# Kernel optimization log

Measured on AMD Instinct MI355X. Metric: run time of the kernel, lower is better.

## Reference

```python
import jax, jax.numpy as jnp
import numpy as np

NB_HEAD = 8
SIZE_PER_HEAD = 32
KEY_SIZE = 32
RATE = 2


def extract_seq_patches(x, kernel_size, rate):
    # x: [B, N, d] -> [B, N, kernel_size, d], dilated local windows (stride=rate)
    B, N, d = x.shape
    k_size = kernel_size + (rate - 1) * (kernel_size - 1)
    p_right = (k_size - 1) // 2
    p_left = k_size - 1 - p_right
    xp = jnp.pad(x, ((0, 0), (p_left, p_right), (0, 0)))
    xs = [xp[:, i:i + N] for i in range(0, k_size, rate)]  # kernel_size slices
    return jnp.stack(xs, axis=2)


def setup_inputs() -> dict:
    key = jax.random.key(0)
    k1, k2, k3 = jax.random.split(key, 3)
    B, S, D = 4, 2046, 256
    x = jax.random.normal(k1, (B, S, D), dtype=jnp.float32)
    # scale like nn.Linear init so softmax logits are well-conditioned
    W = jax.random.normal(k2, (D, NB_HEAD * SIZE_PER_HEAD), dtype=jnp.float32) / np.sqrt(D)
    b = jax.random.normal(k3, (NB_HEAD * SIZE_PER_HEAD,), dtype=jnp.float32) * 0.01
    return {"x": x, "W": W, "b": b}


def reference(x, W, b):
    rate, heads, dk, dv = RATE, NB_HEAD, KEY_SIZE, SIZE_PER_HEAD
    B, S, D = x.shape
    pad_len = rate - S % rate
    xp = jnp.pad(x, ((0, 0), (0, pad_len), (0, 0)))
    N = S + pad_len
    m = N // rate
    qkv = xp @ W + b                 # same Linear used for Q, K, V in the original
    Q = K = V = qkv                  # [B, N, heads*dk]
    ksz = 1 + 2 * (rate - 1)
    kwp = extract_seq_patches(K, ksz, rate)   # [B, N, ksz, H*dk]
    vwp = extract_seq_patches(V, ksz, rate)
    qw = Q.reshape(B, m, rate, heads, dk).transpose(0, 3, 2, 1, 4)   # [B,H,r,m,dk]
    kw = K.reshape(B, m, rate, heads, dk).transpose(0, 3, 2, 1, 4)
    vw = V.reshape(B, m, rate, heads, dv).transpose(0, 3, 2, 1, 4)
    kwp = kwp.reshape(B, m, rate, ksz, heads, dk).transpose(0, 4, 2, 1, 3, 5)  # [B,H,r,m,ksz,dk]
    vwp = vwp.reshape(B, m, rate, ksz, heads, dv).transpose(0, 4, 2, 1, 3, 5)
    scale = 1.0 / np.sqrt(dk).astype(np.float32)
    # strided scores; original transposes the last two dims (a.permute(0,1,2,4,3))
    a = jnp.einsum('bhrid,bhrjd->bhrji', qw, kw) * scale             # [B,H,r,m,m]
    # local-window scores: qw (as length-1 query) against dilated patches
    ap = jnp.einsum('bhrid,bhrikd->bhrik', qw, kwp) * scale          # [B,H,r,m,ksz]
    A = jax.nn.softmax(jnp.concatenate([a, ap], axis=-1), axis=-1)
    a, ap = A[..., :m], A[..., m:]
    o1 = jnp.einsum('bhrij,bhrjd->bhrid', a, vw)                     # [B,H,r,m,dv]
    o2 = jnp.einsum('bhrik,bhrikd->bhrid', ap, vwp)
    o = (o1 + o2).transpose(0, 3, 2, 1, 4).reshape(B, N, heads * dv)
    return o[:, :-pad_len]
```

## Files before the change

### kernel.cpp

```cpp
#include <hip/hip_runtime.h>
#include <stdint.h>
#include <stddef.h>

#define NB_HEAD 8
#define DHEAD   32
#define B_      4
#define S_      2046
#define N_      2048
#define M_      1024
#define D_      256

#define WT_S    264

typedef __attribute__((ext_vector_type(8))) short short8;
typedef __attribute__((ext_vector_type(4))) float f32x4;

__device__ __forceinline__ void bf2x2(uint32_t u, float& lo, float& hi) {
    union { uint32_t i; float f; } a, b;
    a.i = u << 16;
    b.i = u & 0xffff0000u;
    lo = a.f; hi = b.f;
}
__device__ __forceinline__ uint16_t f2bf(float f) {
    union { float f; uint32_t i; } v; v.f = f;
    uint32_t u = v.i;
    u += 0x7fffu + ((u >> 16) & 1u);
    return (uint16_t)(u >> 16);
}
__device__ __forceinline__ short8 ld_frag(const uint16_t* p) {
    union { uint4 u; short8 s; } v;
    v.u = *(const uint4*)p;
    return v.s;
}
__device__ __forceinline__ void unp8(short8 v, float* f) {
    union { short8 s; uint32_t u[4]; } x; x.s = v;
    #pragma unroll
    for (int k = 0; k < 4; ++k) bf2x2(x.u[k], f[2*k], f[2*k+1]);
}
__device__ __forceinline__ uint32_t pkbf(uint32_t hi, uint32_t lo) {
    return __builtin_amdgcn_perm(hi, lo, 0x07060302u);
}

__global__ __launch_bounds__(512) void proj_kernel(
    const float* __restrict__ x, const float* __restrict__ W,
    const float* __restrict__ bias,
    uint16_t* __restrict__ qkv, uint16_t* __restrict__ qkvT)
{
    __shared__ __align__(16) uint16_t WtL[64 * WT_S];
    __shared__ float    mrgP[4][16][64];
    __shared__ uint16_t Tl[64 * 80];
    const int tid  = threadIdx.x;
    const int w    = tid >> 6;
    const int lane = tid & 63;
    const int q    = lane >> 4;
    const int n16  = lane & 15;
    const int rp   = w & 3;
    const int kh   = w >> 2;
    const int rg   = blockIdx.x >> 2;
    const int cg   = blockIdx.x & 3;
    const int n0   = rg * 64;
    const int b    = n0 >> 11;
    const int nnb  = n0 & 2047;
    const int c0   = cg * 64;

    {
        const uint32_t* Wb = (const uint32_t*)(W + c0 + lane);
        #pragma unroll 4
        for (int s = 0; s < 16; ++s) {
            const int k0 = 2 * (w * 16 + s);
            uint32_t a = Wb[(size_t)k0 * D_];
            uint32_t c = Wb[(size_t)(k0 + 1) * D_];
            *(uint32_t*)(WtL + (size_t)lane * WT_S + k0) =
                pkbf(c + 0x8000u, a + 0x8000u);
        }
    }

    const f32x4 kZ = {0.f, 0.f, 0.f, 0.f};
    f32x4 acc[4];
    #pragma unroll
    for (int nt = 0; nt < 4; ++nt) acc[nt] = kZ;

    const int nrow = nnb + rp * 16 + n16;
    const bool ok  = (nrow < S_);
    const float* xrow = x + ((size_t)b * S_ + (ok ? nrow : 0)) * D_;

    __syncthreads();

    #pragma unroll
    for (int kc = 0; kc < 4; ++kc) {
        const int k0 = kh * 128 + kc * 32;
        short8 A;
        if (ok) {
            const uint32_t* xp2 = (const uint32_t*)(xrow + k0 + q * 8);
            uint4 f0 = *(const uint4*)xp2;
            uint4 f1 = *(const uint4*)(xp2 + 4);
            union { uint32_t u[4]; short8 s; } av;
            av.u[0] = pkbf(f0.y + 0x8000u, f0.x + 0x8000u);
            av.u[1] = pkbf(f0.w + 0x8000u, f0.z + 0x8000u);
            av.u[2] = pkbf(f1.y + 0x8000u, f1.x + 0x8000u);
            av.u[3] = pkbf(f1.w + 0x8000u, f1.z + 0x8000u);
            A = av.s;
        } else {
            A = short8{0,0,0,0,0,0,0,0};
        }
        #pragma unroll
        for (int nt = 0; nt < 4; ++nt) {
            short8 Bf = ld_frag(WtL + (size_t)(nt * 16 + n16) * WT_S + k0 + q * 8);
            acc[nt] = __builtin_amdgcn_mfma_f32_16x16x32_bf16(A, Bf, acc[nt], 0, 0, 0);
        }
    }

    if (kh == 1) {
        #pragma unroll
        for (int nt = 0; nt < 4; ++nt)
            #pragma unroll
            for (int r = 0; r < 4; ++r)
                mrgP[rp][nt * 4 + r][lane] = acc[nt][r];
    }
    __syncthreads();
    if (kh == 0) {
        #pragma unroll
        for (int nt = 0; nt < 4; ++nt) {
            const float bv = bias[c0 + nt * 16 + n16];
            #pragma unroll
            for (int r = 0; r < 4; ++r) {
                float v = acc[nt][r] + mrgP[rp][nt * 4 + r][lane] + bv;
                Tl[(rp * 16 + q * 4 + r) * 80 + nt * 16 + n16] = f2bf(v);
            }
        }
    }
    __syncthreads();

    if (w < 4) {
        const int hloc = w >> 1, rr = w & 1;
        const int hglob = (c0 >> 5) + hloc;
        const int pglob = (b * NB_HEAD + hglob) * 2 + rr;
        const int ibase = nnb >> 1;
        uint16_t* qk = qkv  + (size_t)pglob * (M_ * DHEAD);
        uint16_t* qt = qkvT + (size_t)pglob * (M_ * DHEAD);

        {
            const int ii = lane >> 1, d0 = (lane & 1) * 16;
            const uint4* src = (const uint4*)(Tl + (2 * ii + rr) * 80 + hloc * 32 + d0);
            uint4 v0 = src[0], v1 = src[1];
            uint4* dst = (uint4*)(qk + (size_t)(ibase + ii) * DHEAD + d0);
            dst[0] = v0; dst[1] = v1;
        }
        {
            const int d = lane >> 1, ph = (lane & 1) * 16;
            uint32_t pk[8];
            #pragma unroll
            for (int t = 0; t < 16; ++t) {
                const int pos = ph + t;
                const int il = (((pos >> 2) & 1) << 4) | (((pos >> 3) & 3) << 2) | (pos & 3);
                const uint32_t vv = Tl[(2 * il + rr) * 80 + hloc * 32 + d];
                if (t & 1) pk[t >> 1] |= vv << 16; else pk[t >> 1] = vv;
            }
            uint4* dst = (uint4*)(qt + (size_t)d * M_ + ibase + ph);
            dst[0] = *(uint4*)&pk[0];
            dst[1] = *(uint4*)&pk[4];
        }
    }
}

__global__ __launch_bounds__(512) void attn_kernel(
    const uint16_t* __restrict__ qkv, const uint16_t* __restrict__ qkvT,
    float* __restrict__ out)
{
    const float SCL = 0.17677669529663687f * 1.4426950408889634f;
    __shared__ float mrg[4][18][64];
    const int tid  = threadIdx.x;
    const int w    = tid >> 6;
    const int lane = tid & 63;
    const int q    = lane >> 4;
    const int n16  = lane & 15;
    const int rowgrp = w & 3;
    const int jh     = w >> 2;
    const int bid  = blockIdx.x;
    const int p     = ((bid & 7) << 3) | ((bid >> 3) & 7);
    const int chunk = bid >> 6;
    const uint16_t* Xp = qkv  + (size_t)p * (M_ * DHEAD);
    const uint16_t* Xt = qkvT + (size_t)p * (M_ * DHEAD);

    const int rbase = chunk * 128 + rowgrp * 32;
    const int jb0   = jh * 512;
    const f32x4 kZ = {0.f, 0.f, 0.f, 0.f};
    short8 ONES;
    #pragma unroll
    for (int k = 0; k < 8; ++k) ONES[k] = (short)0x3F80;

    short8 Q0 = ld_frag(Xp + (size_t)(rbase + n16) * DHEAD + q * 8);
    short8 Q1 = ld_frag(Xp + (size_t)(rbase + 16 + n16) * DHEAD + q * 8);

    short8 Q0s, Q1s;
    {
        float f0[8], f1[8];
        unp8(Q0, f0); unp8(Q1, f1);
        union { uint16_t h[8]; short8 s; } a, b;
        #pragma unroll
        for (int k = 0; k < 8; ++k) {
            a.h[k] = f2bf(f0[k] * SCL);
            b.h[k] = f2bf(f1[k] * SCL);
        }
        Q0s = a.s; Q1s = b.s;
    }

    f32x4 Ot[2][2];
    #pragma unroll
    for (int it = 0; it < 2; ++it) { Ot[it][0] = kZ; Ot[it][1] = kZ; }
    f32x4 Lacc[2] = {kZ, kZ};

    short8 Bf[4], XF[2][2];
    #pragma unroll
    for (int g = 0; g < 4; ++g)
        Bf[g] = ld_frag(Xp + (size_t)(jb0 + g * 16 + n16) * DHEAD + q * 8);
    #pragma unroll
    for (int h = 0; h < 2; ++h)
        #pragma unroll
        for (int c = 0; c < 2; ++c)
            XF[h][c] = ld_frag(Xt + (size_t)(h * 16 + n16) * M_ + jb0 + c * 32 + q * 8);

    for (int tile = 0; tile < 8; ++tile) {
        f32x4 S0[4], S1[4];
        #pragma unroll
        for (int g = 0; g < 4; ++g) {
            S0[g] = __builtin_amdgcn_mfma_f32_16x16x32_bf16(Bf[g], Q0s, kZ, 0, 0, 0);
            S1[g] = __builtin_amdgcn_mfma_f32_16x16x32_bf16(Bf[g], Q1s, kZ, 0, 0, 0);
        }
        const int jb2 = jb0 + ((tile + 1) & 7) * 64;
        short8 Bn[4], XFn[2][2];
        #pragma unroll
        for (int g = 0; g < 4; ++g)
            Bn[g] = ld_frag(Xp + (size_t)(jb2 + g * 16 + n16) * DHEAD + q * 8);
        #pragma unroll
        for (int h = 0; h < 2; ++h)
            #pragma unroll
            for (int c = 0; c < 2; ++c)
                XFn[h][c] = ld_frag(Xt + (size_t)(h * 16 + n16) * M_ + jb2 + c * 32 + q * 8);

        #pragma unroll
        for (int it = 0; it < 2; ++it) {
            f32x4* S = it ? S1 : S0;
            uint32_t t[4][4];
            #pragma unroll
            for (int g = 0; g < 4; ++g)
                #pragma unroll
                for (int r = 0; r < 4; ++r)
                    t[g][r] = __float_as_uint(exp2f(S[g][r]));
            #pragma unroll
            for (int c = 0; c < 2; ++c) {
                union { uint32_t u[4]; short8 s; } bp;
                bp.u[0] = pkbf(t[2*c][1],   t[2*c][0]);
                bp.u[1] = pkbf(t[2*c][3],   t[2*c][2]);
                bp.u[2] = pkbf(t[2*c+1][1], t[2*c+1][0]);
                bp.u[3] = pkbf(t[2*c+1][3], t[2*c+1][2]);
                Ot[it][0] = __builtin_amdgcn_mfma_f32_16x16x32_bf16(XF[0][c], bp.s, Ot[it][0], 0, 0, 0);
                Ot[it][1] = __builtin_amdgcn_mfma_f32_16x16x32_bf16(XF[1][c], bp.s, Ot[it][1], 0, 0, 0);
                Lacc[it]  = __builtin_amdgcn_mfma_f32_16x16x32_bf16(ONES,     bp.s, Lacc[it],  0, 0, 0);
            }
        }
        #pragma unroll
        for (int g = 0; g < 4; ++g) Bf[g] = Bn[g];
        #pragma unroll
        for (int h = 0; h < 2; ++h) {
            XF[h][0] = XFn[h][0]; XF[h][1] = XFn[h][1];
        }
    }

    float Lp[2] = {Lacc[0][0], Lacc[1][0]};

    if (jh == 1) {
        #pragma unroll
        for (int it = 0; it < 2; ++it)
            #pragma unroll
            for (int h = 0; h < 2; ++h)
                #pragma unroll
                for (int r = 0; r < 4; ++r)
                    mrg[rowgrp][it * 8 + h * 4 + r][lane] = Ot[it][h][r];
        mrg[rowgrp][16][lane] = Lp[0];
        mrg[rowgrp][17][lane] = Lp[1];
    }
    __syncthreads();
    if (jh == 1) return;

    #pragma unroll
    for (int it = 0; it < 2; ++it) {
        #pragma unroll
        for (int h = 0; h < 2; ++h)
            #pragma unroll
            for (int r = 0; r < 4; ++r)
                Ot[it][h][r] += mrg[rowgrp][it * 8 + h * 4 + r][lane];
        Lp[it] += mrg[rowgrp][16 + it][lane];
    }

    const int rpar  = p & 1;
    const int hh    = (p >> 1) & 7;
    const int bglob = p >> 4;

    #pragma unroll
    for (int it = 0; it < 2; ++it) {
        const int i = rbase + it * 16 + n16;
        float qs[8], qr[8];
        unp8(it ? Q1s : Q0s, qs);
        unp8(it ? Q1  : Q0,  qr);
        const int im1 = max(i - 1, 0);
        const int ip1 = min(i + 1, M_ - 1);

        float fm[8], fp[8];
        unp8(ld_frag(Xp + (size_t)im1 * DHEAD + q * 8), fm);
        unp8(ld_frag(Xp + (size_t)ip1 * DHEAD + q * 8), fp);
        float sm = 0.f, s0 = 0.f, sp = 0.f;
        #pragma unroll
        for (int jj = 0; jj < 8; ++jj) {
            sm = fmaf(qs[jj], fm[jj], sm);
            s0 = fmaf(qs[jj], qr[jj], s0);
            sp = fmaf(qs[jj], fp[jj], sp);
        }
        sm += __shfl_xor(sm, 16, 64); sm += __shfl_xor(sm, 32, 64);
        s0 += __shfl_xor(s0, 16, 64); s0 += __shfl_xor(s0, 32, 64);
        sp += __shfl_xor(sp, 16, 64); sp += __shfl_xor(sp, 32, 64);

        const bool vOK = (i > 0), wOK = (i < M_ - 1);
        const float em = vOK ? exp2f(sm) : 1.0f;
        const float e0 = exp2f(s0);
        const float ep = wOK ? exp2f(sp) : 1.0f;
        const float vm = vOK ? em : 0.f;
        const float vp = wOK ? ep : 0.f;
        const float inv = 1.0f / (Lp[it] + em + e0 + ep);

        if (i < M_ - 1) {
            const size_t rowb = ((size_t)bglob * S_ + 2 * i + rpar) * D_ + hh * DHEAD;
            #pragma unroll
            for (int h = 0; h < 2; ++h) {
                float xm[4], x0[4], xp4[4];
                {
                    uint2 u = *(const uint2*)(Xp + (size_t)im1 * DHEAD + h * 16 + q * 4);
                    bf2x2(u.x, xm[0], xm[1]); bf2x2(u.y, xm[2], xm[3]);
                }
                {
                    uint2 u = *(const uint2*)(Xp + (size_t)i * DHEAD + h * 16 + q * 4);
                    bf2x2(u.x, x0[0], x0[1]); bf2x2(u.y, x0[2], x0[3]);
                }
                {
                    uint2 u = *(const uint2*)(Xp + (size_t)ip1 * DHEAD + h * 16 + q * 4);
                    bf2x2(u.x, xp4[0], xp4[1]); bf2x2(u.y, xp4[2], xp4[3]);
                }
                float4 res;
                #pragma unroll
                for (int r = 0; r < 4; ++r) {
                    float v = Ot[it][h][r] + vm * xm[r] + e0 * x0[r] + vp * xp4[r];
                    ((float*)&res)[r] = v * inv;
                }
                *(float4*)(out + rowb + h * 16 + q * 4) = res;
            }
        }
    }
}

extern "C" void kernel_launch(void* const* d_in, const int* in_sizes, int n_in,
                              void* d_out, int out_size, void* d_ws, size_t ws_size,
                              hipStream_t stream) {
    const float* x    = (const float*)d_in[0];
    const float* W    = (const float*)d_in[1];
    const float* bias = (const float*)d_in[2];
    uint16_t* qkv  = (uint16_t*)d_ws;
    uint16_t* qkvT = (uint16_t*)d_ws + (size_t)64 * M_ * DHEAD;
    float* out = (float*)d_out;

    hipLaunchKernelGGL(proj_kernel, dim3(512), dim3(512), 0, stream,
                       x, W, bias, qkv, qkvT);
    hipLaunchKernelGGL(attn_kernel, dim3(512), dim3(512), 0, stream,
                       qkv, qkvT, out);
}
```

Baseline: 97.50 us.

## Fuse projection and attention into a cooperative kernel with a grid sync

A small pre-kernel now converts W to transposed bf16 once. The projection and attention phases run in a single cooperative kernel separated by a grid-wide barrier, and the shared-memory W staging in the projection is dropped in favour of direct global fragment loads. The aim is to remove the per-block W transpose and the launch gap between the two kernels. The cost is a grid sync, an extra small launch, and lower occupancy headroom. If the cooperative launch fails it falls back to two launches.

```diff
diff --git a/kernel.cpp b/kernel.cpp
--- a/kernel.cpp
+++ b/kernel.cpp
@@ -1,6 +1,9 @@
 #include <hip/hip_runtime.h>
+#include <hip/hip_cooperative_groups.h>
 #include <stdint.h>
 #include <stddef.h>
+
+namespace cg = cooperative_groups;
 
 #define NB_HEAD 8
 #define DHEAD   32
@@ -10,8 +13,6 @@
 #define M_      1024
 #define D_      256
 
-#define WT_S    264
-
 typedef __attribute__((ext_vector_type(8))) short short8;
 typedef __attribute__((ext_vector_type(4))) float f32x4;
 
@@ -41,41 +42,44 @@
     return __builtin_amdgcn_perm(hi, lo, 0x07060302u);
 }
 
-__global__ __launch_bounds__(512) void proj_kernel(
-    const float* __restrict__ x, const float* __restrict__ W,
+#define SM_BYTES 26624
+#define OFF_TL   16384
+
+__global__ __launch_bounds__(256) void wt_kernel(
+    const float* __restrict__ W, uint16_t* __restrict__ Wt)
+{
+    const int t  = blockIdx.x * 256 + threadIdx.x;
+    const int c  = t >> 6;
+    const int k0 = (t & 63) * 4;
+    union { uint16_t h[4]; uint2 u; } v;
+    #pragma unroll
+    for (int kk = 0; kk < 4; ++kk)
+        v.h[kk] = f2bf(W[(size_t)(k0 + kk) * D_ + c]);
+    *(uint2*)(Wt + (size_t)c * D_ + k0) = v.u;
+}
+
+__device__ __forceinline__ void proj_phase(
+    const float* __restrict__ x, const uint16_t* __restrict__ Wt,
     const float* __restrict__ bias,
-    uint16_t* __restrict__ qkv, uint16_t* __restrict__ qkvT)
-{
-    __shared__ __align__(16) uint16_t WtL[64 * WT_S];
-    __shared__ float    mrgP[4][16][64];
-    __shared__ uint16_t Tl[64 * 80];
-    const int tid  = threadIdx.x;
+    uint16_t* __restrict__ qkv, uint16_t* __restrict__ qkvT,
+    char* smem, int bid, int tid)
+{
+    float (*mrgP)[16][64] = (float(*)[16][64])smem;
+    uint16_t* Tl = (uint16_t*)(smem + OFF_TL);
+    const f32x4 kZ = {0.f, 0.f, 0.f, 0.f};
     const int w    = tid >> 6;
     const int lane = tid & 63;
     const int q    = lane >> 4;
     const int n16  = lane & 15;
     const int rp   = w & 3;
     const int kh   = w >> 2;
-    const int rg   = blockIdx.x >> 2;
-    const int cg   = blockIdx.x & 3;
+    const int rg   = bid >> 2;
+    const int cgc  = bid & 3;
     const int n0   = rg * 64;
     const int b    = n0 >> 11;
     const int nnb  = n0 & 2047;
-    const int c0   = cg * 64;
-
-    {
-        const uint32_t* Wb = (const uint32_t*)(W + c0 + lane);
-        #pragma unroll 4
-        for (int s = 0; s < 16; ++s) {
-            const int k0 = 2 * (w * 16 + s);
-            uint32_t a = Wb[(size_t)k0 * D_];
-            uint32_t c = Wb[(size_t)(k0 + 1) * D_];
-            *(uint32_t*)(WtL + (size_t)lane * WT_S + k0) =
-                pkbf(c + 0x8000u, a + 0x8000u);
-        }
-    }
-
-    const f32x4 kZ = {0.f, 0.f, 0.f, 0.f};
+    const int c0   = cgc * 64;
+
     f32x4 acc[4];
     #pragma unroll
     for (int nt = 0; nt < 4; ++nt) acc[nt] = kZ;
@@ -83,8 +87,6 @@
     const int nrow = nnb + rp * 16 + n16;
     const bool ok  = (nrow < S_);
     const float* xrow = x + ((size_t)b * S_ + (ok ? nrow : 0)) * D_;
-
-    __syncthreads();
 
     #pragma unroll
     for (int kc = 0; kc < 4; ++kc) {
@@ -105,7 +107,7 @@
         }
         #pragma unroll
         for (int nt = 0; nt < 4; ++nt) {
-            short8 Bf = ld_frag(WtL + (size_t)(nt * 16 + n16) * WT_S + k0 + q * 8);
+            short8 Bf = ld_frag(Wt + (size_t)(c0 + nt * 16 + n16) * D_ + k0 + q * 8);
             acc[nt] = __builtin_amdgcn_mfma_f32_16x16x32_bf16(A, Bf, acc[nt], 0, 0, 0);
         }
     }
@@ -163,20 +165,19 @@
     }
 }
 
-__global__ __launch_bounds__(512) void attn_kernel(
+__device__ __forceinline__ void attn_phase(
     const uint16_t* __restrict__ qkv, const uint16_t* __restrict__ qkvT,
-    float* __restrict__ out)
+    float* __restrict__ out, char* smem, int bid, int tid)
 {
     const float SCL = 0.17677669529663687f * 1.4426950408889634f;
-    __shared__ float mrg[4][18][64];
-    const int tid  = threadIdx.x;
+    float (*mrg)[18][64] = (float(*)[18][64])smem;
+    const f32x4 kZ = {0.f, 0.f, 0.f, 0.f};
     const int w    = tid >> 6;
     const int lane = tid & 63;
     const int q    = lane >> 4;
     const int n16  = lane & 15;
     const int rowgrp = w & 3;
     const int jh     = w >> 2;
-    const int bid  = blockIdx.x;
     const int p     = ((bid & 7) << 3) | ((bid >> 3) & 7);
     const int chunk = bid >> 6;
     const uint16_t* Xp = qkv  + (size_t)p * (M_ * DHEAD);
@@ -184,7 +185,6 @@
 
     const int rbase = chunk * 128 + rowgrp * 32;
     const int jb0   = jh * 512;
-    const f32x4 kZ = {0.f, 0.f, 0.f, 0.f};
     short8 ONES;
     #pragma unroll
     for (int k = 0; k < 8; ++k) ONES[k] = (short)0x3F80;
@@ -281,80 +281,110 @@
         mrg[rowgrp][17][lane] = Lp[1];
     }
     __syncthreads();
-    if (jh == 1) return;
-
-    #pragma unroll
-    for (int it = 0; it < 2; ++it) {
-        #pragma unroll
-        for (int h = 0; h < 2; ++h)
-            #pragma unroll
-            for (int r = 0; r < 4; ++r)
-                Ot[it][h][r] += mrg[rowgrp][it * 8 + h * 4 + r][lane];
-        Lp[it] += mrg[rowgrp][16 + it][lane];
-    }
-
-    const int rpar  = p & 1;
-    const int hh    = (p >> 1) & 7;
-    const int bglob = p >> 4;
-
-    #pragma unroll
-    for (int it = 0; it < 2; ++it) {
-        const int i = rbase + it * 16 + n16;
-        float qs[8], qr[8];
-        unp8(it ? Q1s : Q0s, qs);
-        unp8(it ? Q1  : Q0,  qr);
-        const int im1 = max(i - 1, 0);
-        const int ip1 = min(i + 1, M_ - 1);
-
-        float fm[8], fp[8];
-        unp8(ld_frag(Xp + (size_t)im1 * DHEAD + q * 8), fm);
-        unp8(ld_frag(Xp + (size_t)ip1 * DHEAD + q * 8), fp);
-        float sm = 0.f, s0 = 0.f, sp = 0.f;
-        #pragma unroll
-        for (int jj = 0; jj < 8; ++jj) {
-            sm = fmaf(qs[jj], fm[jj], sm);
-            s0 = fmaf(qs[jj], qr[jj], s0);
-            sp = fmaf(qs[jj], fp[jj], sp);
-        }
-        sm += __shfl_xor(sm, 16, 64); sm += __shfl_xor(sm, 32, 64);
-        s0 += __shfl_xor(s0, 16, 64); s0 += __shfl_xor(s0, 32, 64);
-        sp += __shfl_xor(sp, 16, 64); sp += __shfl_xor(sp, 32, 64);
-
-        const bool vOK = (i > 0), wOK = (i < M_ - 1);
-        const float em = vOK ? exp2f(sm) : 1.0f;
-        const float e0 = exp2f(s0);
-        const float ep = wOK ? exp2f(sp) : 1.0f;
-        const float vm = vOK ? em : 0.f;
-        const float vp = wOK ? ep : 0.f;
-        const float inv = 1.0f / (Lp[it] + em + e0 + ep);
-
-        if (i < M_ - 1) {
-            const size_t rowb = ((size_t)bglob * S_ + 2 * i + rpar) * D_ + hh * DHEAD;
-            #pragma unroll
-            for (int h = 0; h < 2; ++h) {
-                float xm[4], x0[4], xp4[4];
-                {
-                    uint2 u = *(const uint2*)(Xp + (size_t)im1 * DHEAD + h * 16 + q * 4);
-                    bf2x2(u.x, xm[0], xm[1]); bf2x2(u.y, xm[2], xm[3]);
+
+    if (jh == 0) {
+        #pragma unroll
+        for (int it = 0; it < 2; ++it) {
+            #pragma unroll
+            for (int h = 0; h < 2; ++h)
+                #pragma unroll
+                for (int r = 0; r < 4; ++r)
+                    Ot[it][h][r] += mrg[rowgrp][it * 8 + h * 4 + r][lane];
+            Lp[it] += mrg[rowgrp][16 + it][lane];
+        }
+
+        const int rpar  = p & 1;
+        const int hh    = (p >> 1) & 7;
+        const int bglob = p >> 4;
+
+        #pragma unroll
+        for (int it = 0; it < 2; ++it) {
+            const int i = rbase + it * 16 + n16;
+            float qs[8], qr[8];
+            unp8(it ? Q1s : Q0s, qs);
+            unp8(it ? Q1  : Q0,  qr);
+            const int im1 = max(i - 1, 0);
+            const int ip1 = min(i + 1, M_ - 1);
+
+            float fm[8], fp[8];
+            unp8(ld_frag(Xp + (size_t)im1 * DHEAD + q * 8), fm);
+            unp8(ld_frag(Xp + (size_t)ip1 * DHEAD + q * 8), fp);
+            float sm = 0.f, s0 = 0.f, sp = 0.f;
+            #pragma unroll
+            for (int jj = 0; jj < 8; ++jj) {
+                sm = fmaf(qs[jj], fm[jj], sm);
+                s0 = fmaf(qs[jj], qr[jj], s0);
+                sp = fmaf(qs[jj], fp[jj], sp);
+            }
+            sm += __shfl_xor(sm, 16, 64); sm += __shfl_xor(sm, 32, 64);
+            s0 += __shfl_xor(s0, 16, 64); s0 += __shfl_xor(s0, 32, 64);
+            sp += __shfl_xor(sp, 16, 64); sp += __shfl_xor(sp, 32, 64);
+
+            const bool vOK = (i > 0), wOK = (i < M_ - 1);
+            const float em = vOK ? exp2f(sm) : 1.0f;
+            const float e0 = exp2f(s0);
+            const float ep = wOK ? exp2f(sp) : 1.0f;
+            const float vm = vOK ? em : 0.f;
+            const float vp = wOK ? ep : 0.f;
+            const float inv = 1.0f / (Lp[it] + em + e0 + ep);
+
+            if (i < M_ - 1) {
+                const size_t rowb = ((size_t)bglob * S_ + 2 * i + rpar) * D_ + hh * DHEAD;
+                #pragma unroll
+                for (int h = 0; h < 2; ++h) {
+                    float xm[4], x0[4], xp4[4];
+                    {
+                        uint2 u = *(const uint2*)(Xp + (size_t)im1 * DHEAD + h * 16 + q * 4);
+                        bf2x2(u.x, xm[0], xm[1]); bf2x2(u.y, xm[2], xm[3]);
+                    }
+                    {
+                        uint2 u = *(const uint2*)(Xp + (size_t)i * DHEAD + h * 16 + q * 4);
+                        bf2x2(u.x, x0[0], x0[1]); bf2x2(u.y, x0[2], x0[3]);
+                    }
+                    {
+                        uint2 u = *(const uint2*)(Xp + (size_t)ip1 * DHEAD + h * 16 + q * 4);
+                        bf2x2(u.x, xp4[0], xp4[1]); bf2x2(u.y, xp4[2], xp4[3]);
+                    }
+                    float4 res;
+                    #pragma unroll
+                    for (int r = 0; r < 4; ++r) {
+                        float v = Ot[it][h][r] + vm * xm[r] + e0 * x0[r] + vp * xp4[r];
+                        ((float*)&res)[r] = v * inv;
+                    }
+                    *(float4*)(out + rowb + h * 16 + q * 4) = res;
                 }
-                {
-                    uint2 u = *(const uint2*)(Xp + (size_t)i * DHEAD + h * 16 + q * 4);
-                    bf2x2(u.x, x0[0], x0[1]); bf2x2(u.y, x0[2], x0[3]);
-                }
-                {
-                    uint2 u = *(const uint2*)(Xp + (size_t)ip1 * DHEAD + h * 16 + q * 4);
-                    bf2x2(u.x, xp4[0], xp4[1]); bf2x2(u.y, xp4[2], xp4[3]);
-                }
-                float4 res;
-                #pragma unroll
-                for (int r = 0; r < 4; ++r) {
-                    float v = Ot[it][h][r] + vm * xm[r] + e0 * x0[r] + vp * xp4[r];
-                    ((float*)&res)[r] = v * inv;
-                }
-                *(float4*)(out + rowb + h * 16 + q * 4) = res;
             }
         }
     }
+}
+
+__global__ __launch_bounds__(512, 4) void fused_kernel(
+    const float* __restrict__ x, const uint16_t* __restrict__ Wt,
+    const float* __restrict__ bias,
+    uint16_t* __restrict__ qkv, uint16_t* __restrict__ qkvT,
+    float* __restrict__ out)
+{
+    __shared__ __align__(16) char smem[SM_BYTES];
+    proj_phase(x, Wt, bias, qkv, qkvT, smem, blockIdx.x, threadIdx.x);
+    __threadfence();
+    cg::this_grid().sync();
+    attn_phase(qkv, qkvT, out, smem, blockIdx.x, threadIdx.x);
+}
+
+__global__ __launch_bounds__(512, 4) void proj_kernel(
+    const float* __restrict__ x, const uint16_t* __restrict__ Wt,
+    const float* __restrict__ bias,
+    uint16_t* __restrict__ qkv, uint16_t* __restrict__ qkvT)
+{
+    __shared__ __align__(16) char smem[SM_BYTES];
+    proj_phase(x, Wt, bias, qkv, qkvT, smem, blockIdx.x, threadIdx.x);
+}
+__global__ __launch_bounds__(512, 4) void attn_kernel(
+    const uint16_t* __restrict__ qkv, const uint16_t* __restrict__ qkvT,
+    float* __restrict__ out)
+{
+    __shared__ __align__(16) char smem[18432];
+    attn_phase(qkv, qkvT, out, smem, blockIdx.x, threadIdx.x);
 }
 
 extern "C" void kernel_launch(void* const* d_in, const int* in_sizes, int n_in,
@@ -365,10 +395,21 @@
     const float* bias = (const float*)d_in[2];
     uint16_t* qkv  = (uint16_t*)d_ws;
     uint16_t* qkvT = (uint16_t*)d_ws + (size_t)64 * M_ * DHEAD;
+    uint16_t* Wt   = qkvT + (size_t)64 * M_ * DHEAD;
     float* out = (float*)d_out;
 
-    hipLaunchKernelGGL(proj_kernel, dim3(512), dim3(512), 0, stream,
-                       x, W, bias, qkv, qkvT);
-    hipLaunchKernelGGL(attn_kernel, dim3(512), dim3(512), 0, stream,
-                       qkv, qkvT, out);
-}
+    hipLaunchKernelGGL(wt_kernel, dim3(64), dim3(256), 0, stream, W, Wt);
+
+    const uint16_t* Wtc = Wt;
+    void* args[] = { (void*)&x, (void*)&Wtc, (void*)&bias,
+                     (void*)&qkv, (void*)&qkvT, (void*)&out };
+    hipError_t err = hipLaunchCooperativeKernel((const void*)fused_kernel,
+                                                dim3(512), dim3(512),
+                                                args, 0, stream);
+    if (err != hipSuccess) {
+        hipLaunchKernelGGL(proj_kernel, dim3(512), dim3(512), 0, stream,
+                           x, Wt, bias, qkv, qkvT);
+        hipLaunchKernelGGL(attn_kernel, dim3(512), dim3(512), 0, stream,
+                           qkv, qkvT, out);
+    }
+}
```

New measurement: 275.0 us. 182% more time.
